# Optimization experiments

Measured on AMD Instinct MI355X. Metric: run time of the kernel, lower is better.

The kernel has to match this reference:

```python
import jax, jax.numpy as jnp
import numpy as np

H = 128   # render_height
W = 128   # render_width
N = 128   # primitives per frame (from view(B,128,12,2))
K = 12    # control points / polygon vertices per primitive
SOFT = 0.01  # fallback_softness of DiffRasterizer


def setup_inputs() -> dict:
    key = jax.random.key(0)
    k1, k2, k3, k4, k5 = jax.random.split(key, 5)
    T, B = 192, 1
    # state = [3072 control-point coords in [0,1] | 128 aliveness logits]
    trajectory = jax.random.uniform(k1, (T, B, N * K * 2 + N), dtype=jnp.float32)
    colors = jax.random.uniform(k2, (B, N, 3), dtype=jnp.float32)
    alpha = jax.random.uniform(k3, (N,), dtype=jnp.float32)
    z = jax.random.normal(k4, (N,), dtype=jnp.float32)
    csg = jax.random.randint(k5, (N,), 0, 2) > 0
    return {"trajectory": trajectory, "colors": colors, "alpha": alpha, "z": z, "csg": csg}


def _raster(P, c, alpha, alive, z, csg, gx, gy):
    """Soft differentiable rasterizer (fallback path).
    P: [N,K,2] polygon control points in [0,1]; c: [N,3]; alpha/alive/z: [N]; csg: [N] bool.
    Coverage: product of per-edge half-plane sigmoids (soft convex polygon),
    orientation-corrected via shoelace sign. Composited back-to-front by z;
    CSG-subtract primitives erase (occlude) without contributing color.
    """
    v0 = P                                   # [N,K,2]
    v1 = jnp.roll(P, -1, axis=1)             # [N,K,2]
    e = v1 - v0                              # edge vectors
    area2 = jnp.sum(v0[..., 0] * v1[..., 1] - v1[..., 0] * v0[..., 1], axis=1)  # [N]
    orient = jax.lax.stop_gradient(jnp.sign(area2))[:, None]                    # [N,1]
    # signed edge tests for every pixel: [H,W,N,K]
    s = e[..., 0] * (gy[:, :, None, None] - v0[..., 1]) \
      - e[..., 1] * (gx[:, :, None, None] - v0[..., 0])
    cov = jnp.prod(jax.nn.sigmoid(s * orient / SOFT), axis=-1)  # [H,W,N]
    a = cov * alpha * jax.nn.sigmoid(alive)                     # per-primitive alpha
    order = jnp.argsort(z)                                      # back-to-front
    a = a[..., order]
    c = c[order]
    sub = csg[order].astype(a.dtype)
    one_m = 1.0 - a
    # exclusive reverse cumulative transmittance T_i = prod_{j>i}(1 - a_j)
    t_acc = jnp.flip(jnp.cumprod(jnp.flip(one_m, -1), -1), -1)
    t_excl = jnp.concatenate([t_acc[..., 1:], jnp.ones_like(t_acc[..., :1])], -1)
    w = a * t_excl * (1.0 - sub)             # [H,W,N]
    return jnp.einsum('hwn,nc->hwc', w, c)   # [H,W,3]


def reference(trajectory, colors, alpha, z, csg):
    T, B, _ = trajectory.shape
    ys = (jnp.arange(H, dtype=jnp.float32) + 0.5) / H
    xs = (jnp.arange(W, dtype=jnp.float32) + 0.5) / W
    gy, gx = jnp.meshgrid(ys, xs, indexing='ij')  # [H,W]

    def frame(state_t):  # state_t: [B, 3200]
        P = state_t[:, :N * K * 2].reshape(B, N, K, 2)
        alive = state_t[:, N * K * 2:].reshape(B, N)
        return jax.vmap(lambda Pb, cb, ab: _raster(Pb, cb, alpha, ab, z, csg, gx, gy))(P, colors, alive)

    video = jax.lax.map(jax.checkpoint(frame), trajectory)  # [T,B,H,W,3]
    return jnp.transpose(video, (1, 0, 2, 3, 4))            # [B,T,H,W,3]
```

## Files before the change

### kernel.cpp

```cpp
#include <hip/hip_runtime.h>


#define HH 128
#define WW 128
#define NN 128
#define KK 12
#define STPB 1024
#define RTPB 256
#define STATE_SZ (NN * KK * 2 + NN)
#define CULL_U 15.0f
#define COEF_STRIDE 40

typedef float f2 __attribute__((ext_vector_type(2)));

__global__ __launch_bounds__(STPB) void setup_kernel(
    const float* __restrict__ traj,
    const float* __restrict__ colors,
    const float* __restrict__ alpha,
    const float* __restrict__ zval,
    const void*  __restrict__ csg_raw,
    float* __restrict__ g_coef,
    int* __restrict__ g_cnt,
    unsigned char* __restrict__ g_list)
{
    __shared__ __align__(16) float s_coef[NN][COEF_STRIDE];
    __shared__ __align__(16) float2 s_pq[NN][KK];
    __shared__ float s_state[STATE_SZ];
    __shared__ float s_orient[NN];
    __shared__ float s_z[NN];
    __shared__ int   s_slot2prim[NN];
    __shared__ int   s_npos[NN], s_nneg[NN];
    __shared__ unsigned long long s_qbits[HH][4][2];
    __shared__ unsigned char s_list[4 * (HH / 2)][NN];
    __shared__ int s_cnt[4 * (HH / 2)];
    __shared__ int s_mode;

    const int frame = blockIdx.x;
    const int tid   = threadIdx.x;
    const float* st = traj + (size_t)frame * STATE_SZ;

    for (int i = tid; i < STATE_SZ; i += STPB) s_state[i] = st[i];
    if (tid < NN) { s_z[tid] = zval[tid]; s_npos[tid] = 0; s_nneg[tid] = 0; }
    if (tid == 0) {
        const unsigned char* b = (const unsigned char*)csg_raw;
        const unsigned int*  w = (const unsigned int*)csg_raw;
        int mode = 0;
        bool words01 = true;
        for (int i = 0; i < 32; i++) if (w[i] > 1u) { words01 = false; break; }
        if (!words01) {
            bool bytes01 = true;
            for (int i = 0; i < 128; i++) if (b[i] > 1) { bytes01 = false; break; }
            mode = bytes01 ? 1 : 2;
        }
        s_mode = mode;
    }
    __syncthreads();

    if (tid < NN) {
        const int n = tid;
        float area2 = 0.f;
        #pragma unroll
        for (int k = 0; k < KK; k++) {
            int k1 = (k + 1) % KK;
            float v0x = s_state[(n * KK + k)  * 2 + 0];
            float v0y = s_state[(n * KK + k)  * 2 + 1];
            float v1x = s_state[(n * KK + k1) * 2 + 0];
            float v1y = s_state[(n * KK + k1) * 2 + 1];
            area2 += v0x * v1y - v1x * v0y;
        }
        float orient = (area2 > 0.f) ? 1.f : ((area2 < 0.f) ? -1.f : 0.f);
        s_orient[n] = orient;

        float alive = s_state[NN * KK * 2 + n];
        float g = alpha[n] / (1.f + __expf(-alive));

        float zn = s_z[n];
        int rank = 0;
        for (int j = 0; j < NN; j++) {
            float zj = s_z[j];
            rank += (zj < zn || (zj == zn && j < n)) ? 1 : 0;
        }
        int slot = (NN - 1) - rank;
        s_slot2prim[slot] = n;

        int mode = s_mode;
        int sub;
        if (mode == 0)      sub = ((const int*)csg_raw)[n] != 0;
        else if (mode == 1) sub = ((const unsigned char*)csg_raw)[n] != 0;
        else                sub = ((const float*)csg_raw)[n] != 0.f;
        float cs = sub ? 0.f : 1.f;
        s_coef[slot][36] = g;
        s_coef[slot][37] = colors[n * 3 + 0] * cs;
        s_coef[slot][38] = colors[n * 3 + 1] * cs;
        s_coef[slot][39] = colors[n * 3 + 2] * cs;
    }
    __syncthreads();

    const float QSCALE = 100.0f * 1.4426950408889634f;
    for (int idx = tid; idx < NN * KK; idx += STPB) {
        int slot = idx / KK;
        int k    = idx - slot * KK;
        int n    = s_slot2prim[slot];
        int k1   = (k + 1) % KK;
        float v0x = s_state[(n * KK + k)  * 2 + 0];
        float v0y = s_state[(n * KK + k)  * 2 + 1];
        float v1x = s_state[(n * KK + k1) * 2 + 0];
        float v1y = s_state[(n * KK + k1) * 2 + 1];
        float ex = v1x - v0x, ey = v1y - v0y;
        float q  = -s_orient[n] * QSCALE;
        s_coef[slot][0  + k] = q * ex;
        s_coef[slot][12 + k] = -q * ey;
        s_coef[slot][24 + k] = -q * (ex * v0y - ey * v0x);
    }
    __syncthreads();

    const float SLACK = 0.01f;
    for (int idx = tid; idx < NN * KK; idx += STPB) {
        int slot = idx / KK;
        int k    = idx - slot * KK;
        (void)k;
        float A = s_coef[slot][idx - slot * KK];
        float B = s_coef[slot][12 + (idx - slot * KK)];
        float C = s_coef[slot][24 + (idx - slot * KK)];
        float rcpB = __builtin_amdgcn_rcpf(B);
        float Praw = (CULL_U - C) * rcpB;
        float Qraw = -A * rcpB;
        if (B > 0.f) {
            int i = atomicAdd(&s_npos[slot], 1);
            s_pq[slot][i] = make_float2(Qraw, Praw + SLACK);
        } else if (B < 0.f) {
            int i = atomicAdd(&s_nneg[slot], 1);
            s_pq[slot][(KK - 1) - i] = make_float2(-Qraw, -Praw + SLACK);
        } else {
            int i = atomicAdd(&s_nneg[slot], 1);
            s_pq[slot][(KK - 1) - i] = make_float2(0.f, 1e30f);
        }
    }
    __syncthreads();

    const float GX_LO = 0.5f / WW;
    const float GX_HI = (WW - 0.5f) / WW;
    for (int j = 0; j < (HH * NN) / STPB; j++) {
        int idx = j * STPB + tid;
        int r = idx >> 7, s = idx & (NN - 1);
        float gyr = (r + 0.5f) * (1.0f / HH);
        int npos = s_npos[s];
        const float4* pq4 = (const float4*)&s_pq[s][0];
        float y1 = 1e30f, y2 = 1e30f;
        #pragma unroll
        for (int h = 0; h < KK / 2; h++) {
            float4 v = pq4[h];
            int k0 = 2 * h, k1 = 2 * h + 1;
            float t0 = fmaf(v.x, gyr, v.y);
            float t1 = fmaf(v.z, gyr, v.w);
            bool p0 = k0 < npos, p1 = k1 < npos;
            y1 = fminf(y1, p0 ? t0 : 1e30f);
            y2 = fminf(y2, p0 ? 1e30f : t0);
            y1 = fminf(y1, p1 ? t1 : 1e30f);
            y2 = fminf(y2, p1 ? 1e30f : t1);
        }
        float xhi = fminf(y1, GX_HI);
        float xlo = fmaxf(-y2, GX_LO);
        bool ne = (xlo <= xhi);
        #pragma unroll
        for (int q = 0; q < 4; q++) {
            float qlo = (q * 32 + 0.5f) * (1.0f / WW);
            float qhi = (q * 32 + 31.5f) * (1.0f / WW);
            unsigned long long m = __ballot(ne && (xlo <= qhi) && (xhi >= qlo));
            if ((tid & 63) == 0) s_qbits[r][q][(s >= 64) ? 1 : 0] = m;
        }
    }
    __syncthreads();

    if (tid < 4 * (HH / 2)) {
        int rp = tid >> 2, q = tid & 3;
        unsigned long long b0 = s_qbits[2 * rp][q][0] | s_qbits[2 * rp + 1][q][0];
        unsigned long long b1 = s_qbits[2 * rp][q][1] | s_qbits[2 * rp + 1][q][1];
        int n = 0;
        while (b0) { int k = __builtin_ctzll(b0); b0 &= b0 - 1; s_list[tid][n++] = (unsigned char)k; }
        while (b1) { int k = __builtin_ctzll(b1); b1 &= b1 - 1; s_list[tid][n++] = (unsigned char)(64 + k); }
        s_cnt[tid] = n;
    }
    __syncthreads();

    {
        float* dstc = g_coef + (size_t)frame * (NN * COEF_STRIDE);
        const float* srcc = &s_coef[0][0];
        for (int i = tid; i < NN * COEF_STRIDE; i += STPB) dstc[i] = srcc[i];
        if (tid < 256) g_cnt[frame * 256 + tid] = s_cnt[tid];
        unsigned int* dstl = (unsigned int*)(g_list + (size_t)frame * (256 * NN));
        const unsigned int* srcl = (const unsigned int*)&s_list[0][0];
        for (int i = tid; i < (256 * NN) / 4; i += STPB) dstl[i] = srcl[i];
    }
}

struct F3 { float x, y, z; };

__global__ __launch_bounds__(RTPB) void raster_kernel(
    const float* __restrict__ g_coef,
    const int* __restrict__ g_cnt,
    const unsigned char* __restrict__ g_list,
    float* __restrict__ out)
{
    __shared__ unsigned char s_wlist[4][NN];

    const int tid   = threadIdx.x;
    const int wv    = __builtin_amdgcn_readfirstlane(tid >> 6);
    const int lane  = tid & 63;
    const int frame = blockIdx.y;
    const int tile  = blockIdx.x * 4 + wv;
    const int rp    = tile >> 2;
    const int q     = tile & 3;

    const unsigned char* lst = g_list + ((size_t)frame * 256 + tile) * NN;
    if (lane < NN / 4) {
        ((unsigned int*)&s_wlist[wv][0])[lane] = ((const unsigned int*)lst)[lane];
    }
    const int cnt = g_cnt[frame * 256 + tile];

    const int lx  = lane & 31, ly = lane >> 5;
    const int px  = q * 32 + lx;
    const int row = rp * 2 + ly;
    const float gy = (row + 0.5f) * (1.0f / HH);
    const float gx = (px  + 0.5f) * (1.0f / WW);
    const f2 gy2 = {gy, gy};
    const f2 gx2 = {gx, gx};
    const f2 lo2 = {-100.f, -100.f};

    const float* cfr = g_coef + (size_t)frame * (NN * COEF_STRIDE);

    float Tt = 1.f, rr = 0.f, gg = 0.f, bb = 0.f;
    for (int i = 0; i < cnt; i++) {
        int slot = __builtin_amdgcn_readfirstlane((int)s_wlist[wv][i]);
        const float* cf = cfr + slot * COEF_STRIDE;
        const f2* A2 = (const f2*)(cf);
        const f2* B2 = (const f2*)(cf + 12);
        const f2* C2 = (const f2*)(cf + 24);

        f2 qv = {1.f, 1.f};
        #pragma unroll
        for (int j = 0; j < 6; j++) {
            f2 u = __builtin_elementwise_fma(B2[j], gx2,
                     __builtin_elementwise_fma(A2[j], gy2, C2[j]));
            u = __builtin_elementwise_max(u, lo2);
            f2 e;
            e.x = __builtin_amdgcn_exp2f(u.x);
            e.y = __builtin_amdgcn_exp2f(u.y);
            qv = __builtin_elementwise_fma(qv, e, qv);
        }
        float cov = __builtin_amdgcn_rcpf(qv.x * qv.y);

        float a = cov * cf[36];
        float w = a * Tt;
        rr = fmaf(w, cf[37], rr);
        gg = fmaf(w, cf[38], gg);
        bb = fmaf(w, cf[39], bb);
        Tt = fmaf(-a, Tt, Tt);

        if (!__any(Tt > 2e-3f)) break;
    }

    size_t o = ((size_t)frame * (HH * WW) + (size_t)row * WW + px) * 3;
    *(F3*)(out + o) = F3{rr, gg, bb};
}

extern "C" void kernel_launch(void* const* d_in, const int* in_sizes, int n_in,
                              void* d_out, int out_size, void* d_ws, size_t ws_size,
                              hipStream_t stream) {
    const float* traj   = (const float*)d_in[0];
    const float* colors = (const float*)d_in[1];
    const float* alpha  = (const float*)d_in[2];
    const float* zval   = (const float*)d_in[3];
    const void*  csg    = d_in[4];
    float* out = (float*)d_out;

    const int T = in_sizes[0] / STATE_SZ;

    size_t coef_sz = (size_t)T * NN * COEF_STRIDE * sizeof(float);
    size_t cnt_sz  = (size_t)T * 256 * sizeof(int);
    float* g_coef = (float*)d_ws;
    int*   g_cnt  = (int*)((char*)d_ws + coef_sz);
    unsigned char* g_list = (unsigned char*)d_ws + coef_sz + cnt_sz;

    setup_kernel<<<T, STPB, 0, stream>>>(traj, colors, alpha, zval, csg,
                                         g_coef, g_cnt, g_list);
    dim3 grid(256 / 4, T);
    raster_kernel<<<grid, RTPB, 0, stream>>>(g_coef, g_cnt, g_list, out);
}
```

Measured before the change: 208.2 us.

## Process two primitives per raster iteration and restructure setup shared layouts

The raster loop now evaluates two primitives per iteration to expose more independent exp/FMA work, and prefetches the next pair of slot indices. Odd-length lists are padded with a dummy slot 128 whose coefficients are all zero, so it contributes nothing. In setup, the per-edge Q/P tables move to structure-of-arrays, and the tile lists are padded to reduce shared-memory bank conflicts. The trade-off is more registers and an early-exit check that only happens every two primitives.

```diff
diff --git a/kernel.cpp b/kernel.cpp
--- a/kernel.cpp
+++ b/kernel.cpp
@@ -10,6 +10,8 @@
 #define STATE_SZ (NN * KK * 2 + NN)
 #define CULL_U 15.0f
 #define COEF_STRIDE 40
+#define NSLOT (NN + 1)
+#define LISTP 132
 
 typedef float f2 __attribute__((ext_vector_type(2)));
 
@@ -24,15 +26,16 @@
     unsigned char* __restrict__ g_list)
 {
     __shared__ __align__(16) float s_coef[NN][COEF_STRIDE];
-    __shared__ __align__(16) float2 s_pq[NN][KK];
+    __shared__ float sQ[KK][NN];
+    __shared__ float sP[KK][NN];
     __shared__ float s_state[STATE_SZ];
     __shared__ float s_orient[NN];
     __shared__ float s_z[NN];
     __shared__ int   s_slot2prim[NN];
     __shared__ int   s_npos[NN], s_nneg[NN];
     __shared__ unsigned long long s_qbits[HH][4][2];
-    __shared__ unsigned char s_list[4 * (HH / 2)][NN];
-    __shared__ int s_cnt[4 * (HH / 2)];
+    __shared__ unsigned char s_list[256][LISTP];
+    __shared__ int s_cnt[256];
     __shared__ int s_mode;
 
     const int frame = blockIdx.x;
@@ -118,22 +121,21 @@
     for (int idx = tid; idx < NN * KK; idx += STPB) {
         int slot = idx / KK;
         int k    = idx - slot * KK;
-        (void)k;
-        float A = s_coef[slot][idx - slot * KK];
-        float B = s_coef[slot][12 + (idx - slot * KK)];
-        float C = s_coef[slot][24 + (idx - slot * KK)];
+        float A = s_coef[slot][k];
+        float B = s_coef[slot][12 + k];
+        float C = s_coef[slot][24 + k];
         float rcpB = __builtin_amdgcn_rcpf(B);
         float Praw = (CULL_U - C) * rcpB;
         float Qraw = -A * rcpB;
         if (B > 0.f) {
             int i = atomicAdd(&s_npos[slot], 1);
-            s_pq[slot][i] = make_float2(Qraw, Praw + SLACK);
+            sQ[i][slot] = Qraw; sP[i][slot] = Praw + SLACK;
         } else if (B < 0.f) {
             int i = atomicAdd(&s_nneg[slot], 1);
-            s_pq[slot][(KK - 1) - i] = make_float2(-Qraw, -Praw + SLACK);
+            sQ[(KK - 1) - i][slot] = -Qraw; sP[(KK - 1) - i][slot] = -Praw + SLACK;
         } else {
             int i = atomicAdd(&s_nneg[slot], 1);
-            s_pq[slot][(KK - 1) - i] = make_float2(0.f, 1e30f);
+            sQ[(KK - 1) - i][slot] = 0.f; sP[(KK - 1) - i][slot] = 1e30f;
         }
     }
     __syncthreads();
@@ -145,19 +147,13 @@
         int r = idx >> 7, s = idx & (NN - 1);
         float gyr = (r + 0.5f) * (1.0f / HH);
         int npos = s_npos[s];
-        const float4* pq4 = (const float4*)&s_pq[s][0];
         float y1 = 1e30f, y2 = 1e30f;
         #pragma unroll
-        for (int h = 0; h < KK / 2; h++) {
-            float4 v = pq4[h];
-            int k0 = 2 * h, k1 = 2 * h + 1;
-            float t0 = fmaf(v.x, gyr, v.y);
-            float t1 = fmaf(v.z, gyr, v.w);
-            bool p0 = k0 < npos, p1 = k1 < npos;
-            y1 = fminf(y1, p0 ? t0 : 1e30f);
-            y2 = fminf(y2, p0 ? 1e30f : t0);
-            y1 = fminf(y1, p1 ? t1 : 1e30f);
-            y2 = fminf(y2, p1 ? 1e30f : t1);
+        for (int k = 0; k < KK; k++) {
+            float t = fmaf(sQ[k][s], gyr, sP[k][s]);
+            bool p = k < npos;
+            y1 = fminf(y1, p ? t : 1e30f);
+            y2 = fminf(y2, p ? 1e30f : t);
         }
         float xhi = fminf(y1, GX_HI);
         float xlo = fmaxf(-y2, GX_LO);
@@ -172,25 +168,29 @@
     }
     __syncthreads();
 
-    if (tid < 4 * (HH / 2)) {
+    if (tid < 256) {
         int rp = tid >> 2, q = tid & 3;
         unsigned long long b0 = s_qbits[2 * rp][q][0] | s_qbits[2 * rp + 1][q][0];
         unsigned long long b1 = s_qbits[2 * rp][q][1] | s_qbits[2 * rp + 1][q][1];
         int n = 0;
         while (b0) { int k = __builtin_ctzll(b0); b0 &= b0 - 1; s_list[tid][n++] = (unsigned char)k; }
         while (b1) { int k = __builtin_ctzll(b1); b1 &= b1 - 1; s_list[tid][n++] = (unsigned char)(64 + k); }
+        if (n & 1) { s_list[tid][n] = (unsigned char)NN; n++; }
         s_cnt[tid] = n;
     }
     __syncthreads();
 
     {
-        float* dstc = g_coef + (size_t)frame * (NN * COEF_STRIDE);
+        float* dstc = g_coef + (size_t)frame * (NSLOT * COEF_STRIDE);
         const float* srcc = &s_coef[0][0];
         for (int i = tid; i < NN * COEF_STRIDE; i += STPB) dstc[i] = srcc[i];
+        if (tid < COEF_STRIDE) dstc[NN * COEF_STRIDE + tid] = 0.f;
         if (tid < 256) g_cnt[frame * 256 + tid] = s_cnt[tid];
         unsigned int* dstl = (unsigned int*)(g_list + (size_t)frame * (256 * NN));
-        const unsigned int* srcl = (const unsigned int*)&s_list[0][0];
-        for (int i = tid; i < (256 * NN) / 4; i += STPB) dstl[i] = srcl[i];
+        for (int i = tid; i < 256 * (NN / 4); i += STPB) {
+            int row = i >> 5, w = i & 31;
+            dstl[i] = *(const unsigned int*)&s_list[row][w * 4];
+        }
     }
 }
 
@@ -202,7 +202,7 @@
     const unsigned char* __restrict__ g_list,
     float* __restrict__ out)
 {
-    __shared__ unsigned char s_wlist[4][NN];
+    __shared__ unsigned char s_wlist[4][136];
 
     const int tid   = threadIdx.x;
     const int wv    = __builtin_amdgcn_readfirstlane(tid >> 6);
@@ -227,37 +227,57 @@
     const f2 gx2 = {gx, gx};
     const f2 lo2 = {-100.f, -100.f};
 
-    const float* cfr = g_coef + (size_t)frame * (NN * COEF_STRIDE);
+    const float* cfr = g_coef + (size_t)frame * (NSLOT * COEF_STRIDE);
 
     float Tt = 1.f, rr = 0.f, gg = 0.f, bb = 0.f;
-    for (int i = 0; i < cnt; i++) {
-        int slot = __builtin_amdgcn_readfirstlane((int)s_wlist[wv][i]);
-        const float* cf = cfr + slot * COEF_STRIDE;
-        const f2* A2 = (const f2*)(cf);
-        const f2* B2 = (const f2*)(cf + 12);
-        const f2* C2 = (const f2*)(cf + 24);
-
-        f2 qv = {1.f, 1.f};
+
+    int sA = __builtin_amdgcn_readfirstlane((int)s_wlist[wv][0]);
+    int sB = __builtin_amdgcn_readfirstlane((int)s_wlist[wv][1]);
+    for (int i = 0; i < cnt; i += 2) {
+        int sC = __builtin_amdgcn_readfirstlane((int)s_wlist[wv][i + 2]);
+        int sD = __builtin_amdgcn_readfirstlane((int)s_wlist[wv][i + 3]);
+
+        const float* cfA = cfr + sA * COEF_STRIDE;
+        const float* cfB = cfr + sB * COEF_STRIDE;
+
+        f2 qA = {1.f, 1.f}, qB = {1.f, 1.f};
         #pragma unroll
         for (int j = 0; j < 6; j++) {
-            f2 u = __builtin_elementwise_fma(B2[j], gx2,
-                     __builtin_elementwise_fma(A2[j], gy2, C2[j]));
-            u = __builtin_elementwise_max(u, lo2);
-            f2 e;
-            e.x = __builtin_amdgcn_exp2f(u.x);
-            e.y = __builtin_amdgcn_exp2f(u.y);
-            qv = __builtin_elementwise_fma(qv, e, qv);
-        }
-        float cov = __builtin_amdgcn_rcpf(qv.x * qv.y);
-
-        float a = cov * cf[36];
-        float w = a * Tt;
-        rr = fmaf(w, cf[37], rr);
-        gg = fmaf(w, cf[38], gg);
-        bb = fmaf(w, cf[39], bb);
-        Tt = fmaf(-a, Tt, Tt);
+            f2 uA = __builtin_elementwise_fma(((const f2*)(cfA + 12))[j], gx2,
+                      __builtin_elementwise_fma(((const f2*)cfA)[j], gy2,
+                                                ((const f2*)(cfA + 24))[j]));
+            f2 uB = __builtin_elementwise_fma(((const f2*)(cfB + 12))[j], gx2,
+                      __builtin_elementwise_fma(((const f2*)cfB)[j], gy2,
+                                                ((const f2*)(cfB + 24))[j]));
+            uA = __builtin_elementwise_max(uA, lo2);
+            uB = __builtin_elementwise_max(uB, lo2);
+            f2 eA, eB;
+            eA.x = __builtin_amdgcn_exp2f(uA.x);
+            eA.y = __builtin_amdgcn_exp2f(uA.y);
+            eB.x = __builtin_amdgcn_exp2f(uB.x);
+            eB.y = __builtin_amdgcn_exp2f(uB.y);
+            qA = __builtin_elementwise_fma(qA, eA, qA);
+            qB = __builtin_elementwise_fma(qB, eB, qB);
+        }
+        float covA = __builtin_amdgcn_rcpf(qA.x * qA.y);
+        float covB = __builtin_amdgcn_rcpf(qB.x * qB.y);
+
+        float aA = covA * cfA[36];
+        float wA = aA * Tt;
+        rr = fmaf(wA, cfA[37], rr);
+        gg = fmaf(wA, cfA[38], gg);
+        bb = fmaf(wA, cfA[39], bb);
+        Tt = fmaf(-aA, Tt, Tt);
+
+        float aB = covB * cfB[36];
+        float wB = aB * Tt;
+        rr = fmaf(wB, cfB[37], rr);
+        gg = fmaf(wB, cfB[38], gg);
+        bb = fmaf(wB, cfB[39], bb);
+        Tt = fmaf(-aB, Tt, Tt);
 
         if (!__any(Tt > 2e-3f)) break;
+        sA = sC; sB = sD;
     }
 
     size_t o = ((size_t)frame * (HH * WW) + (size_t)row * WW + px) * 3;
@@ -276,7 +296,7 @@
 
     const int T = in_sizes[0] / STATE_SZ;
 
-    size_t coef_sz = (size_t)T * NN * COEF_STRIDE * sizeof(float);
+    size_t coef_sz = (size_t)T * NSLOT * COEF_STRIDE * sizeof(float);
     size_t cnt_sz  = (size_t)T * 256 * sizeof(int);
     float* g_coef = (float*)d_ws;
     int*   g_cnt  = (int*)((char*)d_ws + coef_sz);
```

New measurement: 213.1 us. 1.02x slower.
